# Kernel optimization log

Hardware: AMD Instinct MI355X
Metric: run time of the kernel (lower is better)

## Reference

```python
import jax, jax.numpy as jnp
import numpy as np

B, H, L = 32, 512, 2          # batch, hidden_dim, n_rnn layers per tier
F0 = 128                      # top-tier frame count
UPS = (2, 8)                  # up-sampling factors for tiers 0 and 1
FRAMES = (F0, F0 * UPS[0], F0 * UPS[0] * UPS[1])


def setup_inputs() -> dict:
    key = jax.random.key(0)
    ks = iter(jax.random.split(key, 64))
    k = 1.0 / np.sqrt(H)
    u = lambda shape: jax.random.uniform(next(ks), shape, jnp.float32, -k, k)
    inp = {}
    for t in range(3):
        inp[f"x{t}"] = jax.random.normal(next(ks), (B, FRAMES[t], H), jnp.float32)
    for t in range(3):
        inp[f"Wih{t}"] = u((L, 4 * H, H))
        inp[f"Whh{t}"] = u((L, 4 * H, H))
        inp[f"bih{t}"] = u((L, 4 * H))
        inp[f"bhh{t}"] = u((L, 4 * H))
        inp[f"h0_{t}"] = jax.random.normal(next(ks), (L, B, H), jnp.float32)
        inp[f"c0_{t}"] = jax.random.normal(next(ks), (L, B, H), jnp.float32)
    inp["upW0"] = u((H, UPS[0] * H)); inp["upb0"] = u((UPS[0] * H,))
    inp["upW1"] = u((H, UPS[1] * H)); inp["upb1"] = u((UPS[1] * H,))
    return inp


def _lstm(x, Wih, Whh, bih, bhh, h0, c0):
    # x: (B,T,H); Wih/Whh: (L,4H,H); torch gate order i,f,g,o
    for l in range(L):
        xg = jnp.einsum('bth,gh->btg', x, Wih[l]) + bih[l]  # (B,T,4H)
        Whh_l, bhh_l = Whh[l], bhh[l]

        def step(carry, g_t):
            h, c = carry
            g = g_t + h @ Whh_l.T + bhh_l
            i, f, gg, o = jnp.split(g, 4, axis=-1)
            c = jax.nn.sigmoid(f) * c + jax.nn.sigmoid(i) * jnp.tanh(gg)
            h = jax.nn.sigmoid(o) * jnp.tanh(c)
            return (h, c), h

        _, hs = jax.lax.scan(step, (h0[l], c0[l]), jnp.swapaxes(xg, 0, 1))
        x = jnp.swapaxes(hs, 0, 1)
    return x


def _upsample(x, W, b, t):
    # LinearResampler: Linear(H -> t*H) then unfold time: (B,T,H)->(B,T*t,H)
    Bx, T, Hx = x.shape
    y = x @ W + b  # (B,T,t*H)
    return y.reshape(Bx, T * t, Hx)


def reference(x0, x1, x2,
              Wih0, Whh0, bih0, bhh0, h0_0, c0_0,
              Wih1, Whh1, bih1, bhh1, h0_1, c0_1,
              Wih2, Whh2, bih2, bhh2, h0_2, c0_2,
              upW0, upb0, upW1, upb1):
    h = _lstm(x0, Wih0, Whh0, bih0, bhh0, h0_0, c0_0)
    h = _upsample(h, upW0, upb0, UPS[0])
    h = _lstm(x1 + h, Wih1, Whh1, bih1, bhh1, h0_1, c0_1)
    h = _upsample(h, upW1, upb1, UPS[1])
    h = _lstm(x2 + h, Wih2, Whh2, bih2, bhh2, h0_2, c0_2)
    return h
```

## Files before the change

kernel.cpp:

```cpp
#include <hip/hip_runtime.h>
#include <cstddef>
#include <cstdint>

#define NB 32
#define HD 512
#define GD 2048
#define NL0 32
#define NL1 64
#define FSTR 64
#define NSLOT 8
#define LOSC 0.00048828125f

typedef unsigned short u16;
typedef unsigned int u32;
typedef unsigned long long u64;
typedef _Float16 f16;
typedef __attribute__((ext_vector_type(8))) _Float16 f16x8;
typedef __attribute__((ext_vector_type(4))) float f32x4;

#define MFMAF(a, b, c) __builtin_amdgcn_mfma_f32_16x16x32_f16((a), (b), (c), 0, 0, 0)
#define AT_LD(p)   __hip_atomic_load((p), __ATOMIC_RELAXED, __HIP_MEMORY_SCOPE_AGENT)

#define LDG16(dst, p) \
    asm volatile("global_load_dwordx4 %0, %1, off sc0 sc1" : "=&v"(dst) : "v"(p))
#define ST8(p, v) \
    asm volatile("global_store_dwordx2 %0, %1, off sc0 sc1" :: "v"(p), "v"(v) : "memory")
#define VMCNT0() asm volatile("s_waitcnt vmcnt(0)" ::: "memory")
#define SBAR()   __builtin_amdgcn_sched_barrier(0)

__device__ __forceinline__ float sigf(float x)   { return 1.0f / (1.0f + __expf(-x)); }
__device__ __forceinline__ float tanhf_(float x) { return 2.0f / (1.0f + __expf(-2.0f * x)) - 1.0f; }

__device__ __forceinline__ u16 f2h_bits(float x) {
    f16 h = (f16)x; union { f16 f; u16 u; } c; c.f = h; return c.u;
}
__device__ __forceinline__ float h2f(u16 b) {
    union { u16 u; f16 f; } c; c.u = b; return (float)c.f;
}

__device__ __forceinline__ void cvt8(const float4 a, const float4 b, f16x8& o) {
    o[0] = (f16)a.x; o[1] = (f16)a.y; o[2] = (f16)a.z; o[3] = (f16)a.w;
    o[4] = (f16)b.x; o[5] = (f16)b.y; o[6] = (f16)b.z; o[7] = (f16)b.w;
}
__device__ __forceinline__ void split8f(const float4 a, const float4 b, f16x8& hi, f16x8& lo) {
    float v[8] = {a.x, a.y, a.z, a.w, b.x, b.y, b.z, b.w};
#pragma unroll
    for (int q = 0; q < 8; ++q) {
        const f16 h = (f16)v[q];
        hi[q] = h;
        lo[q] = (f16)((v[q] - (float)h) * 2048.0f);
    }
}

__global__ __launch_bounds__(256) void wsplit_kernel(
    const float* __restrict__ src, u16* __restrict__ hi, u16* __restrict__ lo, int n)
{
    const int i = blockIdx.x * 256 + threadIdx.x;
    if (i < n) {
        const float x = src[i];
        const f16 h = (f16)x;
        union { f16 f; u16 u; } c; c.f = h;
        hi[i] = c.u;
        lo[i] = f2h_bits((x - (float)h) * 2048.0f);
    }
}

__global__ __launch_bounds__(256) void cvtf_kernel(
    const float* __restrict__ src, u16* __restrict__ dst, int n)
{
    const int i = blockIdx.x * 256 + threadIdx.x;
    if (i < n) dst[i] = f2h_bits(src[i]);
}

__global__ __launch_bounds__(256) void addv_kernel(
    const float* __restrict__ a, const float* __restrict__ b, float* __restrict__ o, int n)
{
    const int i = blockIdx.x * 256 + threadIdx.x;
    if (i < n) o[i] = a[i] + b[i];
}

template<int MODE>
__global__ __launch_bounds__(256) void mfma_gemm(
    const float* __restrict__ A, int T, int t0, int tc_bits,
    const float* __restrict__ W, int N,
    const float* __restrict__ b1, const float* __restrict__ b2x,
    float* __restrict__ out, int t_bits, int u_bits)
{
    __shared__ __align__(16) u16 As[64][40], Bh[64][40], Bl[64][40];
    const int tid = threadIdx.x;
    const int m0 = blockIdx.x << 6, n0 = blockIdx.y << 6;

    const int ar = tid >> 2, aks = (tid & 3) << 3;
    const float* aPtr;
    if (MODE == 0) {
        const int rg = m0 + ar;
        const int b = rg >> tc_bits;
        const int tt = t0 + (rg & ((1 << tc_bits) - 1));
        aPtr = A + (((size_t)b * T + tt) << 9) + aks;
    } else {
        aPtr = A + (((size_t)(m0 + ar)) << 9) + aks;
    }
    const float* bPtr = nullptr;
    int bkk = 0, bns = 0;
    if (MODE == 0) {
        bPtr = W + (((size_t)(n0 + ar)) << 9) + aks;
    } else {
        bkk = tid >> 3; bns = (tid & 7) << 3;
        bPtr = W + (size_t)bkk * N + n0 + bns;
    }

    const int lane = tid & 63, wv = tid >> 6;
    const int fr = lane & 15, ko = (lane >> 4) << 3;
    f32x4 acc[4] = {}, accl[4] = {};

    for (int k0 = 0; k0 < HD; k0 += 32) {
        {
            const float4 a1 = *(const float4*)(aPtr + k0);
            const float4 a2 = *(const float4*)(aPtr + k0 + 4);
            f16x8 av; cvt8(a1, a2, av);
            *(f16x8*)&As[ar][aks] = av;
        }
        if (MODE == 0) {
            const float4 w1 = *(const float4*)(bPtr + k0);
            const float4 w2 = *(const float4*)(bPtr + k0 + 4);
            f16x8 vh, vl; split8f(w1, w2, vh, vl);
            *(f16x8*)&Bh[ar][aks] = vh;
            *(f16x8*)&Bl[ar][aks] = vl;
        } else {
            const float4 w1 = *(const float4*)(bPtr + (size_t)k0 * N);
            const float4 w2 = *(const float4*)(bPtr + (size_t)k0 * N + 4);
            f16x8 vh, vl; split8f(w1, w2, vh, vl);
#pragma unroll
            for (int q = 0; q < 8; ++q) {
                union { f16 f; u16 u; } ch, cl; ch.f = vh[q]; cl.f = vl[q];
                Bh[bns + q][bkk] = ch.u;
                Bl[bns + q][bkk] = cl.u;
            }
        }
        __syncthreads();
        const f16x8 ahf = *(const f16x8*)&As[(wv << 4) + fr][ko];
#pragma unroll
        for (int nt = 0; nt < 4; ++nt) {
            const f16x8 bhf = *(const f16x8*)&Bh[(nt << 4) + fr][ko];
            const f16x8 blf = *(const f16x8*)&Bl[(nt << 4) + fr][ko];
            acc[nt]  = MFMAF(ahf, bhf, acc[nt]);
            accl[nt] = MFMAF(ahf, blf, accl[nt]);
        }
        __syncthreads();
    }

    const int mlb = (wv << 4) + ((lane >> 4) << 2);
#pragma unroll
    for (int r = 0; r < 4; ++r) {
        const int mg = m0 + mlb + r;
#pragma unroll
        for (int nt = 0; nt < 4; ++nt) {
            const int n = n0 + (nt << 4) + fr;
            const float v = acc[nt][r] + accl[nt][r] * LOSC;
            if (MODE == 0) {
                out[((size_t)mg << 11) + n] = v + b1[n] + b2x[n];
            } else {
                const int bb = mg >> t_bits, tt = mg & ((1 << t_bits) - 1);
                const int uu = n >> 9, hh = n & 511;
                const size_t di = (((size_t)((((bb << t_bits) + tt) << u_bits) + uu)) << 9) + hh;
                out[di] = v + b1[n] + b2x[di];
            }
        }
    }
}


#define SPIN_WAIT(TGT0, TGT1) do { \
    if (tid < NL0 + NL1) { \
        const int tgt_ = (tid < NL0) ? (TGT0) : (TGT1); \
        if (tgt_ > 0) { \
            const u32* fp_ = flags + tid * FSTR; \
            int g_ = 0; \
            while ((int)AT_LD(fp_) < tgt_ && ++g_ < (1 << 24)) {} \
        } \
    } \
    SBAR(); \
    __syncthreads(); \
} while (0)

__global__ __launch_bounds__(512, 2) void lstm_scan6(
    const float* __restrict__ xg, int Tc,
    const u16* __restrict__ w0h, const u16* __restrict__ w0l,
    const u16* __restrict__ w1ih_h, const u16* __restrict__ w1ih_l,
    const u16* __restrict__ w1hh_h, const u16* __restrict__ w1hh_l,
    const float* __restrict__ bsum1,
    u16* __restrict__ r0, u16* __restrict__ r1,
    float* __restrict__ c0ws, float* __restrict__ c1ws,
    float* __restrict__ out1, int T, int t0, int NS,
    u32* __restrict__ flags)
{
    __shared__ __align__(16) u16 sA[32768];
    __shared__ __align__(16) float sred[16 * 32 * 20];
    __shared__ u16 spk[16][33];
    const int tid = threadIdx.x;
    const int bid = blockIdx.x;
    const int lane = tid & 63, wv = tid >> 6;
    const int kq = wv >> 1, bh = wv & 1;
    const int fr = lane & 15, kg = lane >> 4;
    const int batch = (bh << 4) + fr;
    const int eb = tid & 31;
    const u32 bko = ((u32)batch << 9) + (kq << 7) + (kg << 3);

    if (bid < NL0) {
        const int j0 = bid << 4;
#pragma unroll
        for (int i = 0; i < 8; ++i) {
            const int idx = tid + (i << 9);
            const int hq = idx >> 10, f = (idx >> 6) & 15, l = idx & 63;
            const int lf = l & 15, lk = l >> 4;
            const size_t grow = (((size_t)(lf & 3)) << 9) + j0 + (hq << 2) + (lf >> 2);
            *(f16x8*)&sA[idx << 3] = *(const f16x8*)(w0l + (grow << 9) + (f << 5) + (lk << 3));
        }
        f16x8 Ah_[16];
#pragma unroll
        for (int hq = 0; hq < 4; ++hq) {
            const size_t grow = (((size_t)(fr & 3)) << 9) + j0 + (hq << 2) + (fr >> 2);
#pragma unroll
            for (int ck = 0; ck < 4; ++ck)
                Ah_[(hq << 2) | ck] = *(const f16x8*)(
                    w0h + (grow << 9) + (kq << 7) + (ck << 5) + (kg << 3));
        }
        const int eh = tid >> 5;
        const int hidden = j0 + eh;
        float c_reg = c0ws[((size_t)eb << 9) + hidden];
        __syncthreads();

        for (int jj = 0; jj < Tc; ++jj) {
            const int t = t0 + jj;
            float xv[4];
#pragma unroll
            for (int g = 0; g < 4; ++g)
                xv[g] = xg[(((size_t)eb * Tc + jj) << 11) + (g << 9) + hidden];
            SPIN_WAIT(jj, jj - 6);
            const u16* bp = r0 + (((size_t)((t - 1) & 7)) << 14) + bko;
            f16x8 vb[4];
#pragma unroll
            for (int ck = 0; ck < 4; ++ck)
                LDG16(vb[ck], bp + (ck << 5));
            f16x8 Al_[16];
#pragma unroll
            for (int hq = 0; hq < 4; ++hq)
#pragma unroll
                for (int ck = 0; ck < 4; ++ck)
                    Al_[(hq << 2) | ck] = *(const f16x8*)&sA[
                        ((((hq << 4) + (kq << 2) + ck) << 6) + lane) << 3];
            f32x4 s0[4] = {}, s1[4] = {};
            VMCNT0(); SBAR();
#pragma unroll
            for (int hq = 0; hq < 4; ++hq)
#pragma unroll
                for (int ck = 0; ck < 4; ++ck) {
                    s0[hq] = MFMAF(Ah_[(hq << 2) | ck], vb[ck], s0[hq]);
                    s1[hq] = MFMAF(Al_[(hq << 2) | ck], vb[ck], s1[hq]);
                }
#pragma unroll
            for (int hq = 0; hq < 4; ++hq) {
                const f32x4 sv = s0[hq] + s1[hq] * LOSC;
                const int h16 = (hq << 2) + kg;
                *(f32x4*)&sred[((h16 << 5) + batch) * 20 + (kq << 2)] = sv;
            }
            __syncthreads();
            {
                const int base = ((eh << 5) + eb) * 20;
                const f32x4 q0 = *(const f32x4*)&sred[base];
                const f32x4 q1 = *(const f32x4*)&sred[base + 4];
                const f32x4 q2 = *(const f32x4*)&sred[base + 8];
                const f32x4 q3 = *(const f32x4*)&sred[base + 12];
                const float gi = q0[0] + q1[0] + q2[0] + q3[0] + xv[0];
                const float gf = q0[1] + q1[1] + q2[1] + q3[1] + xv[1];
                const float gg = q0[2] + q1[2] + q2[2] + q3[2] + xv[2];
                const float go = q0[3] + q1[3] + q2[3] + q3[3] + xv[3];
                c_reg = sigf(gf) * c_reg + sigf(gi) * tanhf_(gg);
                const float h = sigf(go) * tanhf_(c_reg);
                spk[eh][eb] = f2h_bits(h);
            }
            __syncthreads();
            if (tid < 128) {
                const int bt = tid & 31, h4 = (tid >> 5) << 2;
                const u64 hp = (u64)spk[h4 + 0][bt] | ((u64)spk[h4 + 1][bt] << 16)
                             | ((u64)spk[h4 + 2][bt] << 32) | ((u64)spk[h4 + 3][bt] << 48);
                const size_t wo = (((size_t)(t & 7)) << 14) + ((size_t)bt << 9) + j0 + h4;
                ST8(r0 + wo, hp);
            }
            VMCNT0();
            __syncthreads();
            if (tid == 0)
                __hip_atomic_store(flags + bid * FSTR, (u32)(jj + 1),
                                   __ATOMIC_RELAXED, __HIP_MEMORY_SCOPE_AGENT);
        }
        c0ws[((size_t)eb << 9) + hidden] = c_reg;
    } else {
        const int j0 = (bid - NL0) << 3;
#pragma unroll
        for (int i = 0; i < 8; ++i) {
            const int idx = tid + (i << 9);
            const int slot = idx >> 10, f = (idx >> 6) & 15, l = idx & 63;
            const int mat = slot >> 1, hq = slot & 1;
            const int lf = l & 15, lk = l >> 4;
            const size_t grow = (((size_t)(lf & 3)) << 9) + j0 + (hq << 2) + (lf >> 2);
            const u16* src = mat ? w1hh_l : w1ih_l;
            *(f16x8*)&sA[idx << 3] = *(const f16x8*)(src + (grow << 9) + (f << 5) + (lk << 3));
        }
        f16x8 Ah_[16];
#pragma unroll
        for (int mat = 0; mat < 2; ++mat)
#pragma unroll
            for (int hq = 0; hq < 2; ++hq) {
                const size_t grow = (((size_t)(fr & 3)) << 9) + j0 + (hq << 2) + (fr >> 2);
                const u16* src = mat ? w1hh_h : w1ih_h;
#pragma unroll
                for (int ck = 0; ck < 4; ++ck)
                    Ah_[(((mat << 1) | hq) << 2) | ck] = *(const f16x8*)(
                        src + (grow << 9) + (kq << 7) + (ck << 5) + (kg << 3));
            }
        const int eh = tid >> 5;
        const int hidden = j0 + (eh & 7);
        float bs[4], c_reg = 0.f;
        if (tid < 256) {
#pragma unroll
            for (int g = 0; g < 4; ++g) bs[g] = bsum1[(g << 9) + hidden];
            c_reg = c1ws[((size_t)eb << 9) + hidden];
        }
        __syncthreads();

        for (int jj = 0; jj < NS; ++jj) {
            const int t = t0 + jj - 1;
            SPIN_WAIT(jj, jj);
            if (t >= 0) {
                const u16* ap = r0 + (((size_t)(t & 7)) << 14) + bko;
                const u16* bp = r1 + (((size_t)((t - 1) & 7)) << 14) + bko;
                f16x8 va[4], vb[4];
#pragma unroll
                for (int ck = 0; ck < 4; ++ck) {
                    LDG16(va[ck], ap + (ck << 5));
                    LDG16(vb[ck], bp + (ck << 5));
                }
                f16x8 Al_[16];
#pragma unroll
                for (int s = 0; s < 4; ++s)
#pragma unroll
                    for (int ck = 0; ck < 4; ++ck)
                        Al_[(s << 2) | ck] = *(const f16x8*)&sA[
                            ((((s << 4) + (kq << 2) + ck) << 6) + lane) << 3];
                f32x4 s0[2] = {}, s1[2] = {};
                VMCNT0(); SBAR();
#pragma unroll
                for (int hq = 0; hq < 2; ++hq)
#pragma unroll
                    for (int ck = 0; ck < 4; ++ck) {
                        const int ia = (hq << 2) | ck;
                        const int ib = ((2 + hq) << 2) | ck;
                        s0[hq] = MFMAF(Ah_[ia], va[ck], s0[hq]);
                        s1[hq] = MFMAF(Al_[ia], va[ck], s1[hq]);
                        s0[hq] = MFMAF(Ah_[ib], vb[ck], s0[hq]);
                        s1[hq] = MFMAF(Al_[ib], vb[ck], s1[hq]);
                    }
#pragma unroll
                for (int hq = 0; hq < 2; ++hq) {
                    const f32x4 sv = s0[hq] + s1[hq] * LOSC;
                    const int h8 = (hq << 2) + kg;
                    *(f32x4*)&sred[((h8 << 5) + batch) * 20 + (kq << 2)] = sv;
                }
            }
            __syncthreads();
            if (t >= 0 && tid < 256) {
                const int base = ((eh << 5) + eb) * 20;
                const f32x4 q0 = *(const f32x4*)&sred[base];
                const f32x4 q1 = *(const f32x4*)&sred[base + 4];
                const f32x4 q2 = *(const f32x4*)&sred[base + 8];
                const f32x4 q3 = *(const f32x4*)&sred[base + 12];
                const float gi = q0[0] + q1[0] + q2[0] + q3[0] + bs[0];
                const float gf = q0[1] + q1[1] + q2[1] + q3[1] + bs[1];
                const float gg = q0[2] + q1[2] + q2[2] + q3[2] + bs[2];
                const float go = q0[3] + q1[3] + q2[3] + q3[3] + bs[3];
                c_reg = sigf(gf) * c_reg + sigf(gi) * tanhf_(gg);
                const float h = sigf(go) * tanhf_(c_reg);
                spk[eh][eb] = f2h_bits(h);
            }
            __syncthreads();
            if (t >= 0 && tid < 64) {
                const int bt = tid & 31, h4 = (tid >> 5) << 2;
                const u64 hp = (u64)spk[h4 + 0][bt] | ((u64)spk[h4 + 1][bt] << 16)
                             | ((u64)spk[h4 + 2][bt] << 32) | ((u64)spk[h4 + 3][bt] << 48);
                const size_t wo = (((size_t)(t & 7)) << 14) + ((size_t)bt << 9) + j0 + h4;
                ST8(r1 + wo, hp);
            }
            VMCNT0();
            __syncthreads();
            if (tid == 0)
                __hip_atomic_store(flags + bid * FSTR, (u32)(jj + 1),
                                   __ATOMIC_RELAXED, __HIP_MEMORY_SCOPE_AGENT);
            if (t >= 0 && tid < 64) {
                const int bt = tid & 31, h4 = (tid >> 5) << 2;
                float4 o;
                o.x = h2f(spk[h4 + 0][bt]);
                o.y = h2f(spk[h4 + 1][bt]);
                o.z = h2f(spk[h4 + 2][bt]);
                o.w = h2f(spk[h4 + 3][bt]);
                *(float4*)(out1 + (((size_t)bt * T + t) << 9) + j0 + h4) = o;
            }
        }
        if (tid < 256) c1ws[((size_t)eb << 9) + hidden] = c_reg;
    }
}

extern "C" void kernel_launch(void* const* d_in, const int* in_sizes, int n_in,
                              void* d_out, int out_size, void* d_ws, size_t ws_size,
                              hipStream_t stream)
{
    const float* x[3]   = {(const float*)d_in[0], (const float*)d_in[1],  (const float*)d_in[2]};
    const float* Wih[3] = {(const float*)d_in[3], (const float*)d_in[9],  (const float*)d_in[15]};
    const float* Whh[3] = {(const float*)d_in[4], (const float*)d_in[10], (const float*)d_in[16]};
    const float* bih[3] = {(const float*)d_in[5], (const float*)d_in[11], (const float*)d_in[17]};
    const float* bhh[3] = {(const float*)d_in[6], (const float*)d_in[12], (const float*)d_in[18]};
    const float* h0[3]  = {(const float*)d_in[7], (const float*)d_in[13], (const float*)d_in[19]};
    const float* c0[3]  = {(const float*)d_in[8], (const float*)d_in[14], (const float*)d_in[20]};
    const float* upW[2] = {(const float*)d_in[21], (const float*)d_in[23]};
    const float* upb[2] = {(const float*)d_in[22], (const float*)d_in[24]};

    float* ws = (float*)d_ws;
    float* bufA  = ws;
    float* bufB  = bufA + (size_t)NB * 256 * HD;
    float* c0ws  = bufB + (size_t)NB * 256 * HD;
    float* c1ws  = c0ws + (size_t)NB * HD;
    float* bsum1 = c1ws + (size_t)NB * HD;
    float* xg    = bsum1 + GD;

    const size_t head_f = 2 * (size_t)NB * 256 * HD + 2 * (size_t)NB * HD + GD;
    const size_t tail_f = 3 * (size_t)GD * HD + NSLOT * (size_t)NB * HD + 96 * FSTR + 64;
    int Tc_cap = 256;
    while (Tc_cap > 32 && (head_f + (size_t)NB * Tc_cap * GD + tail_f) * 4 > ws_size)
        Tc_cap >>= 1;

    u16* w0h    = (u16*)(xg + (size_t)NB * Tc_cap * GD);
    u16* w0l    = w0h + (size_t)GD * HD;
    u16* w1ih_h = w0l + (size_t)GD * HD;
    u16* w1ih_l = w1ih_h + (size_t)GD * HD;
    u16* w1hh_h = w1ih_l + (size_t)GD * HD;
    u16* w1hh_l = w1hh_h + (size_t)GD * HD;
    u16* r0     = w1hh_l + (size_t)GD * HD;
    u16* r1     = r0 + NSLOT * (size_t)NB * HD;
    u32* flags  = (u32*)(r1 + NSLOT * (size_t)NB * HD);

    auto tier = [&](const float* in, float* out1, int T, int tr) {
        const float* Wih0L = Wih[tr];
        const float* Whh0L = Whh[tr];
        const float* Wih1L = Wih[tr] + (size_t)GD * HD;
        const float* Whh1L = Whh[tr] + (size_t)GD * HD;

        wsplit_kernel<<<(GD * HD) / 256, 256, 0, stream>>>(Whh0L, w0h, w0l, GD * HD);
        wsplit_kernel<<<(GD * HD) / 256, 256, 0, stream>>>(Wih1L, w1ih_h, w1ih_l, GD * HD);
        wsplit_kernel<<<(GD * HD) / 256, 256, 0, stream>>>(Whh1L, w1hh_h, w1hh_l, GD * HD);
        addv_kernel<<<GD / 256, 256, 0, stream>>>(bih[tr] + GD, bhh[tr] + GD, bsum1, GD);
        cvtf_kernel<<<(NB * HD) / 256, 256, 0, stream>>>(
            h0[tr], r0 + 7 * (size_t)NB * HD, NB * HD);
        cvtf_kernel<<<(NB * HD) / 256, 256, 0, stream>>>(
            h0[tr] + (size_t)NB * HD, r1 + 7 * (size_t)NB * HD, NB * HD);
        hipMemcpyAsync(c0ws, c0[tr], (size_t)NB * HD * sizeof(float),
                       hipMemcpyDeviceToDevice, stream);
        hipMemcpyAsync(c1ws, c0[tr] + (size_t)NB * HD, (size_t)NB * HD * sizeof(float),
                       hipMemcpyDeviceToDevice, stream);

        const int Tc = T < Tc_cap ? T : Tc_cap;
        int tc_bits = 0; while ((1 << tc_bits) < Tc) ++tc_bits;
        for (int t0 = 0; t0 < T; t0 += Tc) {
            dim3 g((NB * Tc) / 64, GD / 64);
            mfma_gemm<0><<<g, 256, 0, stream>>>(in, T, t0, tc_bits, Wih0L, GD,
                                                bih[tr], bhh[tr], xg, 0, 0);
            hipMemsetAsync(flags, 0, 96 * FSTR * sizeof(u32), stream);
            const bool last = (t0 + Tc >= T);
            const int NS = Tc + (last ? 1 : 0);
            const float* xg_p = xg; int Tc_a = Tc;
            const u16 *a0 = w0h, *a1 = w0l, *a2 = w1ih_h, *a3 = w1ih_l, *a4 = w1hh_h, *a5 = w1hh_l;
            const float* bs_p = bsum1;
            u16 *p0 = r0, *p1 = r1;
            float *c0p = c0ws, *c1p = c1ws, *o1 = out1;
            int T_a = T, t0_a = t0, NS_a = NS;
            u32* fl = flags;
            void* args[] = {(void*)&xg_p, (void*)&Tc_a,
                            (void*)&a0, (void*)&a1, (void*)&a2, (void*)&a3, (void*)&a4, (void*)&a5,
                            (void*)&bs_p, (void*)&p0, (void*)&p1,
                            (void*)&c0p, (void*)&c1p, (void*)&o1,
                            (void*)&T_a, (void*)&t0_a, (void*)&NS_a, (void*)&fl};
            hipLaunchCooperativeKernel((const void*)lstm_scan6, dim3(NL0 + NL1), dim3(512),
                                       args, 0, stream);
        }
    };

    float* dout = (float*)d_out;

    tier(x[0], bufB, 128, 0);
    {
        dim3 g((NB * 128) / 64, 1024 / 64);
        mfma_gemm<1><<<g, 256, 0, stream>>>(bufB, 0, 0, 0, upW[0], 1024,
                                            upb[0], x[1], bufA, 7, 1);
    }
    tier(bufA, bufB, 256, 1);
    {
        dim3 g((NB * 256) / 64, 4096 / 64);
        mfma_gemm<1><<<g, 256, 0, stream>>>(bufB, 0, 0, 0, upW[1], 4096,
                                            upb[1], x[2], dout, 8, 3);
    }
    tier(dout, dout, 2048, 2);
}
```

Before: 11.13 ms.

## Replace flag-based step sync with epoch-tagged hidden-state data polling

Each published fp16 hidden value now carries the low 16 bits of its timestep in the upper half of a 32-bit word. Consumers poll the ring-buffer data directly until every epoch tag matches, so they no longer wait on per-block flags after a store fence and barrier. Layer-1 blocks also start their recurrent (r1) MFMAs before polling for the layer-0 output, which overlaps work with the cross-layer dependency. The cost is twice the ring-buffer traffic per step and extra compare work during polling. Correctness relies on 16-byte stores being seen atomically and on the 16-bit epoch tag never colliding.

```diff
diff --git a/kernel.cpp b/kernel.cpp
--- a/kernel.cpp
+++ b/kernel.cpp
@@ -17,14 +17,15 @@
 typedef _Float16 f16;
 typedef __attribute__((ext_vector_type(8))) _Float16 f16x8;
 typedef __attribute__((ext_vector_type(4))) float f32x4;
+typedef __attribute__((ext_vector_type(4))) unsigned int u32x4;
 
 #define MFMAF(a, b, c) __builtin_amdgcn_mfma_f32_16x16x32_f16((a), (b), (c), 0, 0, 0)
 #define AT_LD(p)   __hip_atomic_load((p), __ATOMIC_RELAXED, __HIP_MEMORY_SCOPE_AGENT)
 
 #define LDG16(dst, p) \
     asm volatile("global_load_dwordx4 %0, %1, off sc0 sc1" : "=&v"(dst) : "v"(p))
-#define ST8(p, v) \
-    asm volatile("global_store_dwordx2 %0, %1, off sc0 sc1" :: "v"(p), "v"(v) : "memory")
+#define ST16(p, v) \
+    asm volatile("global_store_dwordx4 %0, %1, off sc0 sc1" :: "v"(p), "v"(v) : "memory")
 #define VMCNT0() asm volatile("s_waitcnt vmcnt(0)" ::: "memory")
 #define SBAR()   __builtin_amdgcn_sched_barrier(0)
 
@@ -38,10 +39,40 @@
     union { u16 u; f16 f; } c; c.u = b; return (float)c.f;
 }
 
-__device__ __forceinline__ void cvt8(const float4 a, const float4 b, f16x8& o) {
-    o[0] = (f16)a.x; o[1] = (f16)a.y; o[2] = (f16)a.z; o[3] = (f16)a.w;
-    o[4] = (f16)b.x; o[5] = (f16)b.y; o[6] = (f16)b.z; o[7] = (f16)b.w;
-}
+__device__ __forceinline__ f16x8 pack_frag(const u32x4 a, const u32x4 b) {
+    union { u32 u[4]; f16x8 f; } c;
+    c.u[0] = (a[0] & 0xffffu) | (a[1] << 16);
+    c.u[1] = (a[2] & 0xffffu) | (a[3] << 16);
+    c.u[2] = (b[0] & 0xffffu) | (b[1] << 16);
+    c.u[3] = (b[2] & 0xffffu) | (b[3] << 16);
+    return c.f;
+}
+
+#define POLL4(VB, BASE, EPW) do { \
+    u32x4 d_[8]; \
+    int g_ = 0; \
+    for (;;) { \
+        _Pragma("unroll") \
+        for (int ck_ = 0; ck_ < 4; ++ck_) { \
+            LDG16(d_[2 * ck_],     (BASE) + (ck_ << 5)); \
+            LDG16(d_[2 * ck_ + 1], (BASE) + (ck_ << 5) + 4); \
+        } \
+        VMCNT0(); SBAR(); \
+        u32 bad_ = 0; \
+        _Pragma("unroll") \
+        for (int j_ = 0; j_ < 8; ++j_) \
+            _Pragma("unroll") \
+            for (int e_ = 0; e_ < 4; ++e_) \
+                bad_ |= (d_[j_][e_] ^ (EPW)) & 0xffff0000u; \
+        if (__all(bad_ == 0)) break; \
+        if (++g_ > (1 << 20)) break; \
+        __builtin_amdgcn_s_sleep(1); \
+    } \
+    _Pragma("unroll") \
+    for (int ck_ = 0; ck_ < 4; ++ck_) \
+        VB[ck_] = pack_frag(d_[2 * ck_], d_[2 * ck_ + 1]); \
+} while (0)
+
 __device__ __forceinline__ void split8f(const float4 a, const float4 b, f16x8& hi, f16x8& lo) {
     float v[8] = {a.x, a.y, a.z, a.w, b.x, b.y, b.z, b.w};
 #pragma unroll
@@ -50,6 +81,10 @@
         hi[q] = h;
         lo[q] = (f16)((v[q] - (float)h) * 2048.0f);
     }
+}
+__device__ __forceinline__ void cvt8(const float4 a, const float4 b, f16x8& o) {
+    o[0] = (f16)a.x; o[1] = (f16)a.y; o[2] = (f16)a.z; o[3] = (f16)a.w;
+    o[4] = (f16)b.x; o[5] = (f16)b.y; o[6] = (f16)b.z; o[7] = (f16)b.w;
 }
 
 __global__ __launch_bounds__(256) void wsplit_kernel(
@@ -65,11 +100,11 @@
     }
 }
 
-__global__ __launch_bounds__(256) void cvtf_kernel(
-    const float* __restrict__ src, u16* __restrict__ dst, int n)
+__global__ __launch_bounds__(256) void packep_kernel(
+    const float* __restrict__ src, u32* __restrict__ dst, int n, u32 ep)
 {
     const int i = blockIdx.x * 256 + threadIdx.x;
-    if (i < n) dst[i] = f2h_bits(src[i]);
+    if (i < n) dst[i] = (ep << 16) | (u32)f2h_bits(src[i]);
 }
 
 __global__ __launch_bounds__(256) void addv_kernel(
@@ -170,33 +205,20 @@
 }
 
 
-#define SPIN_WAIT(TGT0, TGT1) do { \
-    if (tid < NL0 + NL1) { \
-        const int tgt_ = (tid < NL0) ? (TGT0) : (TGT1); \
-        if (tgt_ > 0) { \
-            const u32* fp_ = flags + tid * FSTR; \
-            int g_ = 0; \
-            while ((int)AT_LD(fp_) < tgt_ && ++g_ < (1 << 24)) {} \
-        } \
-    } \
-    SBAR(); \
-    __syncthreads(); \
-} while (0)
-
-__global__ __launch_bounds__(512, 2) void lstm_scan6(
+__global__ __launch_bounds__(512, 2) void lstm_scan7(
     const float* __restrict__ xg, int Tc,
     const u16* __restrict__ w0h, const u16* __restrict__ w0l,
     const u16* __restrict__ w1ih_h, const u16* __restrict__ w1ih_l,
     const u16* __restrict__ w1hh_h, const u16* __restrict__ w1hh_l,
     const float* __restrict__ bsum1,
-    u16* __restrict__ r0, u16* __restrict__ r1,
+    u32* __restrict__ r0, u32* __restrict__ r1,
     float* __restrict__ c0ws, float* __restrict__ c1ws,
     float* __restrict__ out1, int T, int t0, int NS,
     u32* __restrict__ flags)
 {
     __shared__ __align__(16) u16 sA[32768];
     __shared__ __align__(16) float sred[16 * 32 * 20];
-    __shared__ u16 spk[16][33];
+    __shared__ u32 spk[16][33];
     const int tid = threadIdx.x;
     const int bid = blockIdx.x;
     const int lane = tid & 63, wv = tid >> 6;
@@ -236,12 +258,19 @@
 #pragma unroll
             for (int g = 0; g < 4; ++g)
                 xv[g] = xg[(((size_t)eb * Tc + jj) << 11) + (g << 9) + hidden];
-            SPIN_WAIT(jj, jj - 6);
-            const u16* bp = r0 + (((size_t)((t - 1) & 7)) << 14) + bko;
+            if (tid < NL1) {
+                const int tgt = jj - 6;
+                if (tgt > 0) {
+                    int g_ = 0;
+                    while ((int)AT_LD(flags + tid * FSTR) < tgt && ++g_ < (1 << 22)) {}
+                }
+            }
+            SBAR();
+            __syncthreads();
+            const u32 epw = ((u32)((t - 1) & 0xffff)) << 16;
+            const u32* bp = r0 + (((size_t)((t - 1) & 7)) << 14) + bko;
             f16x8 vb[4];
-#pragma unroll
-            for (int ck = 0; ck < 4; ++ck)
-                LDG16(vb[ck], bp + (ck << 5));
+            POLL4(vb, bp, epw);
             f16x8 Al_[16];
 #pragma unroll
             for (int hq = 0; hq < 4; ++hq)
@@ -250,7 +279,6 @@
                     Al_[(hq << 2) | ck] = *(const f16x8*)&sA[
                         ((((hq << 4) + (kq << 2) + ck) << 6) + lane) << 3];
             f32x4 s0[4] = {}, s1[4] = {};
-            VMCNT0(); SBAR();
 #pragma unroll
             for (int hq = 0; hq < 4; ++hq)
 #pragma unroll
@@ -277,21 +305,16 @@
                 const float go = q0[3] + q1[3] + q2[3] + q3[3] + xv[3];
                 c_reg = sigf(gf) * c_reg + sigf(gi) * tanhf_(gg);
                 const float h = sigf(go) * tanhf_(c_reg);
-                spk[eh][eb] = f2h_bits(h);
+                spk[eh][eb] = (((u32)(t & 0xffff)) << 16) | (u32)f2h_bits(h);
             }
             __syncthreads();
             if (tid < 128) {
                 const int bt = tid & 31, h4 = (tid >> 5) << 2;
-                const u64 hp = (u64)spk[h4 + 0][bt] | ((u64)spk[h4 + 1][bt] << 16)
-                             | ((u64)spk[h4 + 2][bt] << 32) | ((u64)spk[h4 + 3][bt] << 48);
-                const size_t wo = (((size_t)(t & 7)) << 14) + ((size_t)bt << 9) + j0 + h4;
-                ST8(r0 + wo, hp);
-            }
-            VMCNT0();
-            __syncthreads();
-            if (tid == 0)
-                __hip_atomic_store(flags + bid * FSTR, (u32)(jj + 1),
-                                   __ATOMIC_RELAXED, __HIP_MEMORY_SCOPE_AGENT);
+                u32x4 v;
+                v[0] = spk[h4 + 0][bt]; v[1] = spk[h4 + 1][bt];
+                v[2] = spk[h4 + 2][bt]; v[3] = spk[h4 + 3][bt];
+                ST16(r0 + (((size_t)(t & 7)) << 14) + ((size_t)bt << 9) + j0 + h4, v);
+            }
         }
         c0ws[((size_t)eb << 9) + hidden] = c_reg;
     } else {
@@ -330,16 +353,11 @@
 
         for (int jj = 0; jj < NS; ++jj) {
             const int t = t0 + jj - 1;
-            SPIN_WAIT(jj, jj);
             if (t >= 0) {
-                const u16* ap = r0 + (((size_t)(t & 7)) << 14) + bko;
-                const u16* bp = r1 + (((size_t)((t - 1) & 7)) << 14) + bko;
-                f16x8 va[4], vb[4];
-#pragma unroll
-                for (int ck = 0; ck < 4; ++ck) {
-                    LDG16(va[ck], ap + (ck << 5));
-                    LDG16(vb[ck], bp + (ck << 5));
-                }
+                const u32 ep1 = ((u32)((t - 1) & 0xffff)) << 16;
+                const u32* b1p = r1 + (((size_t)((t - 1) & 7)) << 14) + bko;
+                f16x8 vb[4];
+                POLL4(vb, b1p, ep1);
                 f16x8 Al_[16];
 #pragma unroll
                 for (int s = 0; s < 4; ++s)
@@ -348,17 +366,25 @@
                         Al_[(s << 2) | ck] = *(const f16x8*)&sA[
                             ((((s << 4) + (kq << 2) + ck) << 6) + lane) << 3];
                 f32x4 s0[2] = {}, s1[2] = {};
-                VMCNT0(); SBAR();
+#pragma unroll
+                for (int hq = 0; hq < 2; ++hq)
+#pragma unroll
+                    for (int ck = 0; ck < 4; ++ck) {
+                        const int ib = ((2 + hq) << 2) | ck;
+                        s0[hq] = MFMAF(Ah_[ib], vb[ck], s0[hq]);
+                        s1[hq] = MFMAF(Al_[ib], vb[ck], s1[hq]);
+                    }
+                const u32 ep0 = ((u32)(t & 0xffff)) << 16;
+                const u32* b0p = r0 + (((size_t)(t & 7)) << 14) + bko;
+                f16x8 va[4];
+                POLL4(va, b0p, ep0);
 #pragma unroll
                 for (int hq = 0; hq < 2; ++hq)
 #pragma unroll
                     for (int ck = 0; ck < 4; ++ck) {
                         const int ia = (hq << 2) | ck;
-                        const int ib = ((2 + hq) << 2) | ck;
                         s0[hq] = MFMAF(Ah_[ia], va[ck], s0[hq]);
                         s1[hq] = MFMAF(Al_[ia], va[ck], s1[hq]);
-                        s0[hq] = MFMAF(Ah_[ib], vb[ck], s0[hq]);
-                        s1[hq] = MFMAF(Al_[ib], vb[ck], s1[hq]);
                     }
 #pragma unroll
                 for (int hq = 0; hq < 2; ++hq) {
@@ -380,30 +406,29 @@
                 const float go = q0[3] + q1[3] + q2[3] + q3[3] + bs[3];
                 c_reg = sigf(gf) * c_reg + sigf(gi) * tanhf_(gg);
                 const float h = sigf(go) * tanhf_(c_reg);
-                spk[eh][eb] = f2h_bits(h);
+                spk[eh][eb] = (((u32)(t & 0xffff)) << 16) | (u32)f2h_bits(h);
             }
             __syncthreads();
             if (t >= 0 && tid < 64) {
                 const int bt = tid & 31, h4 = (tid >> 5) << 2;
-                const u64 hp = (u64)spk[h4 + 0][bt] | ((u64)spk[h4 + 1][bt] << 16)
-                             | ((u64)spk[h4 + 2][bt] << 32) | ((u64)spk[h4 + 3][bt] << 48);
-                const size_t wo = (((size_t)(t & 7)) << 14) + ((size_t)bt << 9) + j0 + h4;
-                ST8(r1 + wo, hp);
-            }
-            VMCNT0();
-            __syncthreads();
+                u32x4 v;
+                v[0] = spk[h4 + 0][bt]; v[1] = spk[h4 + 1][bt];
+                v[2] = spk[h4 + 2][bt]; v[3] = spk[h4 + 3][bt];
+                ST16(r1 + (((size_t)(t & 7)) << 14) + ((size_t)bt << 9) + j0 + h4, v);
+            }
             if (tid == 0)
-                __hip_atomic_store(flags + bid * FSTR, (u32)(jj + 1),
+                __hip_atomic_store(flags + (bid - NL0) * FSTR, (u32)(jj + 1),
                                    __ATOMIC_RELAXED, __HIP_MEMORY_SCOPE_AGENT);
             if (t >= 0 && tid < 64) {
                 const int bt = tid & 31, h4 = (tid >> 5) << 2;
                 float4 o;
-                o.x = h2f(spk[h4 + 0][bt]);
-                o.y = h2f(spk[h4 + 1][bt]);
-                o.z = h2f(spk[h4 + 2][bt]);
-                o.w = h2f(spk[h4 + 3][bt]);
+                o.x = h2f((u16)(spk[h4 + 0][bt] & 0xffffu));
+                o.y = h2f((u16)(spk[h4 + 1][bt] & 0xffffu));
+                o.z = h2f((u16)(spk[h4 + 2][bt] & 0xffffu));
+                o.w = h2f((u16)(spk[h4 + 3][bt] & 0xffffu));
                 *(float4*)(out1 + (((size_t)bt * T + t) << 9) + j0 + h4) = o;
             }
+            __syncthreads();
         }
         if (tid < 256) c1ws[((size_t)eb << 9) + hidden] = c_reg;
     }
@@ -432,7 +457,7 @@
     float* xg    = bsum1 + GD;
 
     const size_t head_f = 2 * (size_t)NB * 256 * HD + 2 * (size_t)NB * HD + GD;
-    const size_t tail_f = 3 * (size_t)GD * HD + NSLOT * (size_t)NB * HD + 96 * FSTR + 64;
+    const size_t tail_f = 3 * (size_t)GD * HD + 2 * NSLOT * (size_t)NB * HD + NL1 * FSTR + 64;
     int Tc_cap = 256;
     while (Tc_cap > 32 && (head_f + (size_t)NB * Tc_cap * GD + tail_f) * 4 > ws_size)
         Tc_cap >>= 1;
@@ -443,9 +468,9 @@
     u16* w1ih_l = w1ih_h + (size_t)GD * HD;
     u16* w1hh_h = w1ih_l + (size_t)GD * HD;
     u16* w1hh_l = w1hh_h + (size_t)GD * HD;
-    u16* r0     = w1hh_l + (size_t)GD * HD;
-    u16* r1     = r0 + NSLOT * (size_t)NB * HD;
-    u32* flags  = (u32*)(r1 + NSLOT * (size_t)NB * HD);
+    u32* r0     = (u32*)(w1hh_l + (size_t)GD * HD);
+    u32* r1     = r0 + NSLOT * (size_t)NB * HD;
+    u32* flags  = r1 + NSLOT * (size_t)NB * HD;
 
     auto tier = [&](const float* in, float* out1, int T, int tr) {
         const float* Wih0L = Wih[tr];
@@ -457,10 +482,10 @@
         wsplit_kernel<<<(GD * HD) / 256, 256, 0, stream>>>(Wih1L, w1ih_h, w1ih_l, GD * HD);
         wsplit_kernel<<<(GD * HD) / 256, 256, 0, stream>>>(Whh1L, w1hh_h, w1hh_l, GD * HD);
         addv_kernel<<<GD / 256, 256, 0, stream>>>(bih[tr] + GD, bhh[tr] + GD, bsum1, GD);
-        cvtf_kernel<<<(NB * HD) / 256, 256, 0, stream>>>(
-            h0[tr], r0 + 7 * (size_t)NB * HD, NB * HD);
-        cvtf_kernel<<<(NB * HD) / 256, 256, 0, stream>>>(
-            h0[tr] + (size_t)NB * HD, r1 + 7 * (size_t)NB * HD, NB * HD);
+        packep_kernel<<<(NB * HD) / 256, 256, 0, stream>>>(
+            h0[tr], r0 + 7 * (size_t)NB * HD, NB * HD, 0xFFFFu);
+        packep_kernel<<<(NB * HD) / 256, 256, 0, stream>>>(
+            h0[tr] + (size_t)NB * HD, r1 + 7 * (size_t)NB * HD, NB * HD, 0xFFFFu);
         hipMemcpyAsync(c0ws, c0[tr], (size_t)NB * HD * sizeof(float),
                        hipMemcpyDeviceToDevice, stream);
         hipMemcpyAsync(c1ws, c0[tr] + (size_t)NB * HD, (size_t)NB * HD * sizeof(float),
@@ -472,13 +497,13 @@
             dim3 g((NB * Tc) / 64, GD / 64);
             mfma_gemm<0><<<g, 256, 0, stream>>>(in, T, t0, tc_bits, Wih0L, GD,
                                                 bih[tr], bhh[tr], xg, 0, 0);
-            hipMemsetAsync(flags, 0, 96 * FSTR * sizeof(u32), stream);
+            hipMemsetAsync(flags, 0, NL1 * FSTR * sizeof(u32), stream);
             const bool last = (t0 + Tc >= T);
             const int NS = Tc + (last ? 1 : 0);
             const float* xg_p = xg; int Tc_a = Tc;
             const u16 *a0 = w0h, *a1 = w0l, *a2 = w1ih_h, *a3 = w1ih_l, *a4 = w1hh_h, *a5 = w1hh_l;
             const float* bs_p = bsum1;
-            u16 *p0 = r0, *p1 = r1;
+            u32 *p0 = r0, *p1 = r1;
             float *c0p = c0ws, *c1p = c1ws, *o1 = out1;
             int T_a = T, t0_a = t0, NS_a = NS;
             u32* fl = flags;
@@ -487,7 +512,7 @@
                             (void*)&bs_p, (void*)&p0, (void*)&p1,
                             (void*)&c0p, (void*)&c1p, (void*)&o1,
                             (void*)&T_a, (void*)&t0_a, (void*)&NS_a, (void*)&fl};
-            hipLaunchCooperativeKernel((const void*)lstm_scan6, dim3(NL0 + NL1), dim3(512),
+            hipLaunchCooperativeKernel((const void*)lstm_scan7, dim3(NL0 + NL1), dim3(512),
                                        args, 0, stream);
         }
     };
```

After: 15.93 ms. 1.43x slower.
